# Performance work log

Hardware: AMD Instinct MI355X
Metric: run time of the kernel (lower is better)

Reference implementation:

```python
import jax, jax.numpy as jnp
import numpy as np
import math

L_SIDE = 32           # one_side_length = ceil(sqrt(L)), L = 32**2
NDIM = 16             # args.ndim (SSM state size)
N_SSM = 16            # args.n_ssm
DIRS = 4              # args.directions_amount
EMBED = 1024          # embed_dim
KD = DIRS * N_SSM     # kernel_dim = 64
CDIM = EMBED * DIRS   # C_dimensions = 4096
H = EMBED // N_SSM    # 64 (channels per ssm)
R2 = 16               # expansion terms per kernel position
R = L_SIDE * L_SIDE * R2
V = 2 * L_SIDE        # vander power dim (power_dim = kernel_dim_arg*2)
BSZ = 8
SEQ = L_SIDE * L_SIDE


def _build_one_matrix():
    # Mimics CoeffCalculator.whole_as_one: for each of d=2 flow axes and each
    # of R expansion terms, the 4 A-factor rows are one-hot selectors over the
    # V power basis, and the 5th (B) row holds an integer coefficient in one of
    # the first two columns (selecting B1 or B2).
    rng = np.random.default_rng(0)
    M = np.zeros((2, 5, R, V), dtype=np.float32)
    di = np.arange(2)[:, None]
    ri = np.arange(R)[None, :]
    for a in range(4):
        idx = rng.integers(0, V, size=(2, R))
        M[di, a, ri, idx] = 1.0
    col = rng.integers(0, 2, size=(2, R))
    coef = rng.integers(1, 5, size=(2, R)).astype(np.float32)
    M[di, 4, ri, col] = coef
    return jnp.asarray(M)


def setup_inputs() -> dict:
    key = jax.random.key(0)
    ks = jax.random.split(key, 7)
    return {
        "x": jax.random.normal(ks[0], (SEQ, BSZ, EMBED), jnp.float32),
        "A": jax.random.normal(ks[1], (4, KD, NDIM), jnp.float32) * 0.2,
        "B1": jax.random.normal(ks[2], (KD, NDIM), jnp.float32) * 0.2,
        "B2": jax.random.normal(ks[3], (KD, NDIM), jnp.float32) * 0.2,
        "C1": jax.random.normal(ks[4], (CDIM, NDIM), jnp.float32),
        "C2": jax.random.normal(ks[5], (CDIM, NDIM), jnp.float32),
        "omega": jax.random.normal(ks[6], (EMBED,), jnp.float32),
        "one_matrix": _build_one_matrix(),
    }


def _compute_kernel(A, B1, B2, C1, C2, one_matrix, dtype):
    scale = 1.0 / math.sqrt(NDIM)
    # _calc_coeffs: sigmoid on A, B
    As = jax.nn.sigmoid(A)                                  # (4, KD, NDIM)
    pw = jnp.arange(V, dtype=dtype)
    # torch.linalg.vander: increasing powers 0..V-1 -> (4, V, KD, NDIM)
    A_vals = jnp.transpose(As[..., None] ** pw, (0, 3, 1, 2))
    Bs = jax.nn.sigmoid(jnp.stack([B1, B2], 0))             # (2, KD, NDIM)
    Bpad = jnp.zeros((V, KD, NDIM), dtype).at[:2].set(Bs)   # pad to V rows
    vals = jnp.concatenate([A_vals, Bpad[None]], 0)         # (5, V, KD, NDIM)
    # 'd a R V, a V k n -> d a R k n' then product over the 5 factors
    prod = jnp.einsum('drv,vkn->drkn', one_matrix[:, 0], vals[0])
    for a in range(1, 5):
        prod = prod * jnp.einsum('drv,vkn->drkn', one_matrix[:, a], vals[a])
    # sum over r2 expansion terms per kernel position
    w = prod.reshape(2, SEQ, R2, KD, NDIM).sum(2)           # (2, SEQ, KD, NDIM)
    C = jnp.stack([C1, C2], 0) * scale                      # (2, CDIM, NDIM)
    Cr = C.reshape(2, H, KD, NDIM)
    k = jnp.einsum('dpkn,dhkn->phk', w, Cr).reshape(L_SIDE, L_SIDE, CDIM)
    # boundary scaling (first row/col x2, corner net x1)
    k = k.at[0, :, :].multiply(2.0)
    k = k.at[:, 0, :].multiply(2.0)
    k = k.at[0, 0, :].divide(4.0)
    return k


def reference(x, A, B1, B2, C1, C2, omega, one_matrix):
    k = _compute_kernel(A, B1, B2, C1, C2, one_matrix, x.dtype)
    # channel layout (H, dir, n_ssm) -> per-direction (EMBED,) kernels
    kd = k.reshape(L_SIDE, L_SIDE, H, DIRS, N_SSM)
    kd = jnp.transpose(kd, (3, 2, 4, 0, 1)).reshape(DIRS, EMBED, L_SIDE, L_SIDE)
    # 4-corner scans: flip kernel per direction; conv is linear so sum kernels
    ksum = kd[0] + kd[1, :, ::-1, :] + kd[2, :, :, ::-1] + kd[3, :, ::-1, ::-1]
    residual = x * omega                                    # 'L B D, D -> L B D'
    xg = jnp.transpose(x, (1, 2, 0)).reshape(BSZ, EMBED, L_SIDE, L_SIDE)
    s = 2 * L_SIDE
    xf = jnp.fft.rfft2(xg, s=(s, s))                        # (B, D, s, s//2+1)
    kf = jnp.fft.rfft2(ksum, s=(s, s))
    y = jnp.fft.irfft2(xf * kf, s=(s, s))[..., :L_SIDE, :L_SIDE]
    y = jnp.transpose(y.reshape(BSZ, EMBED, SEQ), (2, 0, 1))  # back to (L, B, D)
    return y + residual
```

## Files before the change

kernel.cpp:

```cpp
#include <hip/hip_runtime.h>
#include <stdint.h>


typedef __attribute__((ext_vector_type(8))) short short8;
typedef __attribute__((ext_vector_type(4))) float f32x4;

__device__ inline uint16_t f2bf(float f) {
    uint32_t u = __float_as_uint(f);
    uint32_t r = (u + 0x7FFFu + ((u >> 16) & 1u)) >> 16;
    return (uint16_t)r;
}
__device__ inline float bf2f(uint16_t v) {
    return __uint_as_float((uint32_t)v << 16);
}
__device__ inline uint32_t packbf(float a, float b) {
    return (uint32_t)f2bf(a) | ((uint32_t)f2bf(b) << 16);
}

__global__ __launch_bounds__(256) void k_pre(const float* __restrict__ x,
                                             uint16_t* __restrict__ xtb,
                                             const float* __restrict__ A,
                                             const float* __restrict__ B1,
                                             const float* __restrict__ B2,
                                             float* __restrict__ LAg,
                                             float* __restrict__ SBg) {
    __shared__ __align__(16) float shf[32 * 129];
    int bx = blockIdx.x;
    int t = threadIdx.x;

    if (bx < 2048) {
        int u = bx & 31, e0 = ((bx >> 5) & 31) * 32, r0 = (bx >> 10) * 128;
        {
            int c = t & 7, a = t >> 3;
            const float* src = x + (size_t)(u * 256 + r0) * 1024 + e0 + c * 4;
            #pragma unroll
            for (int qq = 0; qq < 4; ++qq) {
                int r = qq * 32 + a;
                float4 v = *(const float4*)(src + (size_t)r * 1024);
                shf[(c * 4 + 0) * 129 + r] = v.x;
                shf[(c * 4 + 1) * 129 + r] = v.y;
                shf[(c * 4 + 2) * 129 + r] = v.z;
                shf[(c * 4 + 3) * 129 + r] = v.w;
            }
        }
        __syncthreads();
        {
            int e_local = t >> 3, b = t & 7;
            const float* row = shf + e_local * 129;
            int v0 = r0 >> 3;
            uint32_t pk[8];
            #pragma unroll
            for (int k2 = 0; k2 < 8; ++k2)
                pk[k2] = packbf(row[(2 * k2) * 8 + b], row[(2 * k2 + 1) * 8 + b]);
            uint16_t* dst = xtb + (size_t)(e0 + e_local) * 8192 + u * 256 + b * 32 + v0;
            *(uint4*)dst       = make_uint4(pk[0], pk[1], pk[2], pk[3]);
            *(uint4*)(dst + 8) = make_uint4(pk[4], pk[5], pk[6], pk[7]);
        }
    } else {
        int i = bx - 2048;
        int e = t * 4;
        if (i < 4) {
            float4 v = *(const float4*)(A + i * 1024 + e);
            float4 o;
            o.x = -log2f(1.0f + expf(-v.x));
            o.y = -log2f(1.0f + expf(-v.y));
            o.z = -log2f(1.0f + expf(-v.z));
            o.w = -log2f(1.0f + expf(-v.w));
            *(float4*)(LAg + i * 1024 + e) = o;
        } else {
            const float* Bs = (i == 4) ? B1 : B2;
            float4 v = *(const float4*)(Bs + e);
            float4 o;
            o.x = 1.0f / (1.0f + expf(-v.x));
            o.y = 1.0f / (1.0f + expf(-v.y));
            o.z = 1.0f / (1.0f + expf(-v.z));
            o.w = 1.0f / (1.0f + expf(-v.w));
            *(float4*)(SBg + (i - 4) * 1024 + e) = o;
        }
    }
}

__global__ __launch_bounds__(256) void k_w(const float* __restrict__ om,
                                           const float* __restrict__ LAg,
                                           const float* __restrict__ SBg,
                                           float* __restrict__ w) {
    __shared__ float ff[2][16][4];
    __shared__ float cf[2][16][2];
    int p = blockIdx.x;
    int t = threadIdx.x;
    {
        int row_id = t >> 1, h = t & 1;
        int d = row_id >> 6, a = (row_id >> 4) & 3, r2 = row_id & 15;
        const float* src = om + ((size_t)(d * 5 + a) * 16384 + p * 16 + r2) * 64 + h * 32;
        float s = 0.0f;
        #pragma unroll
        for (int q = 0; q < 8; ++q) {
            float4 v = *(const float4*)(src + q * 4);
            float jb = (float)(h * 32 + q * 4);
            s = __builtin_fmaf(v.x, jb,
                __builtin_fmaf(v.y, jb + 1.0f,
                __builtin_fmaf(v.z, jb + 2.0f,
                __builtin_fmaf(v.w, jb + 3.0f, s))));
        }
        s += __shfl_xor(s, 1);
        if (h == 0) ff[d][r2][a] = s;
        if (t < 32) {
            int dd = t >> 4, rr = t & 15;
            const float* c = om + ((size_t)(dd * 5 + 4) * 16384 + p * 16 + rr) * 64;
            cf[dd][rr][0] = c[0];
            cf[dd][rr][1] = c[1];
        }
    }
    __syncthreads();

    int d = t >> 7;
    int j0 = (t & 127) * 8;
    float L0[8], L1[8], L2[8], L3[8], B0v[8], B1v[8], acc[8];
    #pragma unroll
    for (int a = 0; a < 4; ++a) {
        float* La = (a == 0) ? L0 : (a == 1) ? L1 : (a == 2) ? L2 : L3;
        float4 u0 = *(const float4*)(LAg + a * 1024 + j0);
        float4 u1 = *(const float4*)(LAg + a * 1024 + j0 + 4);
        La[0] = u0.x; La[1] = u0.y; La[2] = u0.z; La[3] = u0.w;
        La[4] = u1.x; La[5] = u1.y; La[6] = u1.z; La[7] = u1.w;
    }
    {
        float4 u0 = *(const float4*)(SBg + j0);
        float4 u1 = *(const float4*)(SBg + j0 + 4);
        float4 v0 = *(const float4*)(SBg + 1024 + j0);
        float4 v1 = *(const float4*)(SBg + 1024 + j0 + 4);
        B0v[0] = u0.x; B0v[1] = u0.y; B0v[2] = u0.z; B0v[3] = u0.w;
        B0v[4] = u1.x; B0v[5] = u1.y; B0v[6] = u1.z; B0v[7] = u1.w;
        B1v[0] = v0.x; B1v[1] = v0.y; B1v[2] = v0.z; B1v[3] = v0.w;
        B1v[4] = v1.x; B1v[5] = v1.y; B1v[6] = v1.z; B1v[7] = v1.w;
    }
    #pragma unroll
    for (int jj = 0; jj < 8; ++jj) acc[jj] = 0.0f;

    #pragma unroll
    for (int r2 = 0; r2 < 16; ++r2) {
        float f0 = ff[d][r2][0];
        float f1 = ff[d][r2][1];
        float f2 = ff[d][r2][2];
        float f3 = ff[d][r2][3];
        float c0 = cf[d][r2][0];
        float c1 = cf[d][r2][1];
        #pragma unroll
        for (int jj = 0; jj < 8; ++jj) {
            float ex = __builtin_fmaf(f3, L3[jj],
                       __builtin_fmaf(f2, L2[jj],
                       __builtin_fmaf(f1, L1[jj], f0 * L0[jj])));
            float bs = __builtin_fmaf(c1, B1v[jj], c0 * B0v[jj]);
            acc[jj] = __builtin_fmaf(exp2f(ex), bs, acc[jj]);
        }
    }
    float* dst = w + (size_t)(d * 1024 + p) * 1024 + j0;
    *(float4*)(dst)     = make_float4(acc[0], acc[1], acc[2], acc[3]);
    *(float4*)(dst + 4) = make_float4(acc[4], acc[5], acc[6], acc[7]);
}

__global__ __launch_bounds__(256) void k_kd(const float* __restrict__ w,
                                            const float* __restrict__ C1,
                                            const float* __restrict__ C2,
                                            uint16_t* __restrict__ kd4b) {
    __shared__ float Wl[128 * 33];
    __shared__ float Ctl[32 * 65];
    int kap = blockIdx.x;
    int p0 = blockIdx.y * 128;
    int dir = kap >> 4, m = kap & 15;
    int t = threadIdx.x;

    {
        int off = (t & 3) * 4;
        #pragma unroll
        for (int rep = 0; rep < 4; ++rep) {
            int row_id = rep * 64 + (t >> 2);
            int d = row_id >> 7, pp = row_id & 127;
            const float* src = w + ((size_t)(d * 1024 + p0 + pp) * 64 + kap) * 16 + off;
            float4 v = *(const float4*)src;
            float* dstl = Wl + pp * 33 + d * 16 + off;
            dstl[0] = v.x; dstl[1] = v.y; dstl[2] = v.z; dstl[3] = v.w;
        }
    }
    if (t < 128) {
        int d = t >> 6, h = t & 63;
        const float* Cd = d ? C2 : C1;
        const float* src = Cd + (size_t)(h * 64 + kap) * 16;
        #pragma unroll
        for (int q = 0; q < 16; ++q)
            Ctl[(d * 16 + q) * 65 + h] = src[q] * 0.25f;
    }
    __syncthreads();

    int ph = t & 15, hq = t >> 4;
    int pl = ph * 8, h0 = hq * 4;
    float acc[8][4];
    #pragma unroll
    for (int i = 0; i < 8; ++i)
        { acc[i][0] = acc[i][1] = acc[i][2] = acc[i][3] = 0.0f; }

    for (int k = 0; k < 32; ++k) {
        float c0 = Ctl[k * 65 + h0 + 0];
        float c1 = Ctl[k * 65 + h0 + 1];
        float c2 = Ctl[k * 65 + h0 + 2];
        float c3 = Ctl[k * 65 + h0 + 3];
        #pragma unroll
        for (int i = 0; i < 8; ++i) {
            float wv = Wl[(pl + i) * 33 + k];
            acc[i][0] += wv * c0; acc[i][1] += wv * c1;
            acc[i][2] += wv * c2; acc[i][3] += wv * c3;
        }
    }
    #pragma unroll
    for (int j = 0; j < 4; ++j) {
        int h = h0 + j;
        uint32_t pk[4];
        #pragma unroll
        for (int qq = 0; qq < 4; ++qq) {
            float v0, v1;
            #pragma unroll
            for (int z = 0; z < 2; ++z) {
                int p = p0 + pl + qq * 2 + z;
                int ii = p >> 5, jj = p & 31;
                float f = ((ii == 0) != (jj == 0)) ? 2.0f : 1.0f;
                float val = acc[qq * 2 + z][j] * f;
                if (z == 0) v0 = val; else v1 = val;
            }
            pk[qq] = packbf(v0, v1);
        }
        uint16_t* dst = kd4b + ((size_t)(dir * 1024 + h * 16 + m)) * 1024 + p0 + pl;
        *(uint4*)dst = make_uint4(pk[0], pk[1], pk[2], pk[3]);
    }
}

__global__ __launch_bounds__(256) void k_conv(const uint16_t* __restrict__ xtb,
                                              const uint16_t* __restrict__ kd4b,
                                              uint16_t* __restrict__ ytb) {
    __shared__ __align__(16) char smem[24576 + 16384];
    const int KROW = 768;
    const int SROW = 96;
    char* xtl = smem + 24576;

    int e = blockIdx.x;
    int t = threadIdx.x;
    int lane = t & 63, wv = t >> 6;
    int n = lane & 15, q = lane >> 4, nn = n & 7;

    {
        f32x4 z = {0.f, 0.f, 0.f, 0.f};
        #pragma unroll
        for (int k = 0; k < 6; ++k)
            *(f32x4*)(smem + (t + k * 256) * 16) = z;
    }
    {
        const uint4* src = (const uint4*)(xtb + (size_t)e * 8192);
        #pragma unroll
        for (int r = 0; r < 4; ++r) {
            uint4 v = src[r * 256 + t];
            *(uint4*)(xtl + (r * 256 + t) * 16) = v;
        }
    }
    int pi = t >> 3, pj = (t & 7) * 4;
    float s0, s1, s2, s3;
    {
        const uint16_t* b0 = kd4b + (size_t)e * 1024;
        ushort4 a0 = *(const ushort4*)(b0 + pi * 32 + pj);
        ushort4 a1 = *(const ushort4*)(b0 + (1 << 20) + (31 - pi) * 32 + pj);
        ushort4 a2 = *(const ushort4*)(b0 + (2 << 20) + pi * 32 + (28 - pj));
        ushort4 a3 = *(const ushort4*)(b0 + (3 << 20) + (31 - pi) * 32 + (28 - pj));
        s0 = bf2f(a0.x) + bf2f(a1.x) + bf2f(a2.w) + bf2f(a3.w);
        s1 = bf2f(a0.y) + bf2f(a1.y) + bf2f(a2.z) + bf2f(a3.z);
        s2 = bf2f(a0.z) + bf2f(a1.z) + bf2f(a2.y) + bf2f(a3.y);
        s3 = bf2f(a0.w) + bf2f(a1.w) + bf2f(a2.x) + bf2f(a3.x);
    }
    __syncthreads();

    {
        uint16_t k0 = f2bf(s0), k1 = f2bf(s1), k2 = f2bf(s2), k3 = f2bf(s3);
        #pragma unroll
        for (int s = 0; s < 8; ++s) {
            uint16_t* row = (uint16_t*)(smem + pi * KROW + s * SROW);
            int c = 31 + s - pj;
            row[c]     = k0;
            row[c - 1] = k1;
            row[c - 2] = k2;
            row[c - 3] = k3;
        }
    }
    __syncthreads();

    int A0 = n - 8 * q;
    int A1 = A0 + 16;
    int sh1 = (A1 + 9) & 7;
    int off1 = sh1 * SROW + (31 + sh1 - A1) * 2;
    int off0;
    if (A0 >= -8) {
        int sh0 = (A0 + 9) & 7;
        off0 = sh0 * SROW + (31 + sh0 - A0) * 2;
    } else {
        off0 = 80;
    }
    int boff = nn * 64 + q * 16;

    short8 Breg[16];
    #pragma unroll
    for (int u = 0; u < 16; ++u)
        Breg[u] = *(const short8*)(xtl + u * 512 + boff);

    f32x4 acc0[8], acc1[8];
    #pragma unroll
    for (int ii = 0; ii < 8; ++ii) {
        acc0[ii] = (f32x4){0.f, 0.f, 0.f, 0.f};
        acc1[ii] = (f32x4){0.f, 0.f, 0.f, 0.f};
    }

    #pragma unroll
    for (int dd = 0; dd < 4; ++dd) {
        if (dd <= wv) {
            const char* krow = smem + (wv - dd) * KROW;
            short8 a0 = *(const short8*)(krow + off0);
            short8 a1 = *(const short8*)(krow + off1);
            #pragma unroll
            for (int ii = 0; ii < 8; ++ii) {
                short8 bb = (ii < 4) ? Breg[dd + 4 * ii]
                                     : *(const short8*)(xtl + (dd + 4 * ii) * 512 + boff);
                acc0[ii] = __builtin_amdgcn_mfma_f32_16x16x32_bf16(a0, bb, acc0[ii], 0, 0, 0);
                acc1[ii] = __builtin_amdgcn_mfma_f32_16x16x32_bf16(a1, bb, acc1[ii], 0, 0, 0);
            }
        }
    }
    #pragma unroll
    for (int g = 1; g <= 7; ++g) {
        #pragma unroll
        for (int dd = 0; dd < 4; ++dd) {
            const char* krow = smem + (wv + 4 * g - 3 + dd) * KROW;
            short8 a0 = *(const short8*)(krow + off0);
            short8 a1 = *(const short8*)(krow + off1);
            #pragma unroll
            for (int ii = g; ii < 8; ++ii) {
                int u = 4 * (ii - g) + 3 - dd;
                short8 bb = (ii - g < 4) ? Breg[u]
                                         : *(const short8*)(xtl + u * 512 + boff);
                acc0[ii] = __builtin_amdgcn_mfma_f32_16x16x32_bf16(a0, bb, acc0[ii], 0, 0, 0);
                acc1[ii] = __builtin_amdgcn_mfma_f32_16x16x32_bf16(a1, bb, acc1[ii], 0, 0, 0);
            }
        }
    }

    if (n < 8) {
        uint16_t* base = ytb + ((size_t)(n * 1024 + e)) * 1024 + q * 4;
        #pragma unroll
        for (int ii = 0; ii < 8; ++ii) {
            int i = wv + 4 * ii;
            uint2 w0 = make_uint2(packbf(acc0[ii][0], acc0[ii][1]),
                                  packbf(acc0[ii][2], acc0[ii][3]));
            uint2 w1 = make_uint2(packbf(acc1[ii][0], acc1[ii][1]),
                                  packbf(acc1[ii][2], acc1[ii][3]));
            *(uint2*)(base + i * 32)      = w0;
            *(uint2*)(base + i * 32 + 16) = w1;
        }
    }
}

__global__ __launch_bounds__(256) void k_t2(const uint16_t* __restrict__ ytb,
                                            const float* __restrict__ x,
                                            const float* __restrict__ omega,
                                            float* __restrict__ out) {
    __shared__ float lds[32 * 130];
    int e0 = blockIdx.x * 32, p0 = blockIdx.y * 128, b = blockIdx.z;
    int t = threadIdx.x;
    {
        int a = t >> 3, c = t & 7;
        const uint16_t* src = ytb + (size_t)(b * 1024 + e0 + a) * 1024 + p0;
        float* dst = lds + a * 130;
        #pragma unroll
        for (int rep = 0; rep < 2; ++rep) {
            int off = (c + rep * 8) * 8;
            uint4 v = *(const uint4*)(src + off);
            uint32_t ww[4] = {v.x, v.y, v.z, v.w};
            #pragma unroll
            for (int k = 0; k < 4; ++k) {
                float2 f;
                f.x = bf2f((uint16_t)(ww[k] & 0xFFFFu));
                f.y = bf2f((uint16_t)(ww[k] >> 16));
                *(float2*)(dst + off + k * 2) = f;
            }
        }
    }
    __syncthreads();
    int pl = t >> 1, eh = (t & 1) * 16;
    int p = p0 + pl;
    const float* xs = x + ((size_t)(p * 8 + b)) * 1024 + e0 + eh;
    float* os = out + ((size_t)(p * 8 + b)) * 1024 + e0 + eh;
    #pragma unroll
    for (int qq = 0; qq < 4; ++qq) {
        float4 xv = *(const float4*)(xs + qq * 4);
        int eb = eh + qq * 4;
        float4 ov;
        ov.x = lds[(eb + 0) * 130 + pl] + xv.x * omega[e0 + eb + 0];
        ov.y = lds[(eb + 1) * 130 + pl] + xv.y * omega[e0 + eb + 1];
        ov.z = lds[(eb + 2) * 130 + pl] + xv.z * omega[e0 + eb + 2];
        ov.w = lds[(eb + 3) * 130 + pl] + xv.w * omega[e0 + eb + 3];
        *(float4*)(os + qq * 4) = ov;
    }
}

extern "C" void kernel_launch(void* const* d_in, const int* in_sizes, int n_in,
                              void* d_out, int out_size, void* d_ws, size_t ws_size,
                              hipStream_t stream) {
    (void)in_sizes; (void)n_in; (void)out_size; (void)ws_size;
    const float* x   = (const float*)d_in[0];
    const float* A   = (const float*)d_in[1];
    const float* B1  = (const float*)d_in[2];
    const float* B2  = (const float*)d_in[3];
    const float* C1  = (const float*)d_in[4];
    const float* C2  = (const float*)d_in[5];
    const float* omg = (const float*)d_in[6];
    const float* om  = (const float*)d_in[7];
    float* out = (float*)d_out;

    float* ws  = (float*)d_ws;
    uint16_t* xtb  = (uint16_t*)ws;
    uint16_t* kd4b = (uint16_t*)(ws + 4194304);
    uint16_t* ytb  = (uint16_t*)(ws + 6291456);
    float* w       = ws + 10485760;
    float* LAg     = ws + 4194304 + 65536;
    float* SBg     = ws + 4194304 + 69632;

    k_pre <<<2054, 256, 0, stream>>>(x, xtb, A, B1, B2, LAg, SBg);
    k_w   <<<1024, 256, 0, stream>>>(om, LAg, SBg, w);
    k_kd  <<<dim3(64, 8), 256, 0, stream>>>(w, C1, C2, kd4b);
    k_conv<<<1024, 256, 0, stream>>>(xtb, kd4b, ytb);
    k_t2  <<<dim3(32, 8, 8), 256, 0, stream>>>(ytb, x, omg, out);
}
```

Measured before the change: 189.7 us.

## Pack two output rows per MFMA tile using all 16 columns in conv

Reworks the MFMA mapping in the direct 2D convolution kernel. Each 16-column B tile now carries two output rows, one per half of the lanes (8 batch columns each), where before only 8 of the 16 columns held useful data. This halves the number of accumulators and MFMA calls per wave and removes the register-cached B fragments. In exchange, every B fragment is now read from LDS on each use, with extra pointer selects that substitute a zero row for out-of-range taps.

```diff
diff --git a/kernel.cpp b/kernel.cpp
--- a/kernel.cpp
+++ b/kernel.cpp
@@ -244,7 +244,7 @@
     int e = blockIdx.x;
     int t = threadIdx.x;
     int lane = t & 63, wv = t >> 6;
-    int n = lane & 15, q = lane >> 4, nn = n & 7;
+    int n = lane & 15, q = lane >> 4, nn = n & 7, hi = n >> 3;
 
     {
         f32x4 z = {0.f, 0.f, 0.f, 0.f};
@@ -301,63 +301,68 @@
         off0 = 80;
     }
     int boff = nn * 64 + q * 16;
-
-    short8 Breg[16];
-    #pragma unroll
-    for (int u = 0; u < 16; ++u)
-        Breg[u] = *(const short8*)(xtl + u * 512 + boff);
-
-    f32x4 acc0[8], acc1[8];
-    #pragma unroll
-    for (int ii = 0; ii < 8; ++ii) {
+    const char* zptr = smem + 80;
+
+    f32x4 acc0[4], acc1[4];
+    #pragma unroll
+    for (int ii = 0; ii < 4; ++ii) {
         acc0[ii] = (f32x4){0.f, 0.f, 0.f, 0.f};
         acc1[ii] = (f32x4){0.f, 0.f, 0.f, 0.f};
     }
 
     #pragma unroll
-    for (int dd = 0; dd < 4; ++dd) {
-        if (dd <= wv) {
-            const char* krow = smem + (wv - dd) * KROW;
+    for (int j = 0; j < 8; ++j) {
+        if (j <= 2 * wv + 1) {
+            const char* krow = smem + j * KROW;
             short8 a0 = *(const short8*)(krow + off0);
             short8 a1 = *(const short8*)(krow + off1);
-            #pragma unroll
-            for (int ii = 0; ii < 8; ++ii) {
-                short8 bb = (ii < 4) ? Breg[dd + 4 * ii]
-                                     : *(const short8*)(xtl + (dd + 4 * ii) * 512 + boff);
+            {
+                int u = 2 * wv + hi - j;
+                const char* bp = (u >= 0) ? (xtl + u * 512 + boff) : zptr;
+                short8 bb = *(const short8*)bp;
+                acc0[0] = __builtin_amdgcn_mfma_f32_16x16x32_bf16(a0, bb, acc0[0], 0, 0, 0);
+                acc1[0] = __builtin_amdgcn_mfma_f32_16x16x32_bf16(a1, bb, acc1[0], 0, 0, 0);
+            }
+            #pragma unroll
+            for (int ii = 1; ii < 4; ++ii) {
+                int u = 2 * wv + 8 * ii + hi - j;
+                short8 bb = *(const short8*)(xtl + u * 512 + boff);
                 acc0[ii] = __builtin_amdgcn_mfma_f32_16x16x32_bf16(a0, bb, acc0[ii], 0, 0, 0);
                 acc1[ii] = __builtin_amdgcn_mfma_f32_16x16x32_bf16(a1, bb, acc1[ii], 0, 0, 0);
             }
         }
     }
     #pragma unroll
-    for (int g = 1; g <= 7; ++g) {
-        #pragma unroll
-        for (int dd = 0; dd < 4; ++dd) {
-            const char* krow = smem + (wv + 4 * g - 3 + dd) * KROW;
+    for (int b = 1; b <= 3; ++b) {
+        #pragma unroll
+        for (int m = 0; m < 8; ++m) {
+            int di = 2 * wv + 8 * b - 6 + m;
+            const char* krow = smem + di * KROW;
             short8 a0 = *(const short8*)(krow + off0);
             short8 a1 = *(const short8*)(krow + off1);
             #pragma unroll
-            for (int ii = g; ii < 8; ++ii) {
-                int u = 4 * (ii - g) + 3 - dd;
-                short8 bb = (ii - g < 4) ? Breg[u]
-                                         : *(const short8*)(xtl + u * 512 + boff);
+            for (int ii = b; ii < 4; ++ii) {
+                int u = 8 * (ii - b) + 6 + hi - m;
+                const char* bp = ((ii == b) && (m == 7) && (hi == 0))
+                                     ? zptr : (xtl + u * 512 + boff);
+                short8 bb = *(const short8*)bp;
                 acc0[ii] = __builtin_amdgcn_mfma_f32_16x16x32_bf16(a0, bb, acc0[ii], 0, 0, 0);
                 acc1[ii] = __builtin_amdgcn_mfma_f32_16x16x32_bf16(a1, bb, acc1[ii], 0, 0, 0);
             }
         }
     }
 
-    if (n < 8) {
-        uint16_t* base = ytb + ((size_t)(n * 1024 + e)) * 1024 + q * 4;
-        #pragma unroll
-        for (int ii = 0; ii < 8; ++ii) {
-            int i = wv + 4 * ii;
+    {
+        uint16_t* base = ytb + ((size_t)(nn * 1024 + e)) * 1024 + q * 4;
+        #pragma unroll
+        for (int ii = 0; ii < 4; ++ii) {
+            int ro = 2 * wv + 8 * ii + hi;
             uint2 w0 = make_uint2(packbf(acc0[ii][0], acc0[ii][1]),
                                   packbf(acc0[ii][2], acc0[ii][3]));
             uint2 w1 = make_uint2(packbf(acc1[ii][0], acc1[ii][1]),
                                   packbf(acc1[ii][2], acc1[ii][3]));
-            *(uint2*)(base + i * 32)      = w0;
-            *(uint2*)(base + i * 32 + 16) = w1;
+            *(uint2*)(base + ro * 32)      = w0;
+            *(uint2*)(base + ro * 32 + 16) = w1;
         }
     }
 }
```

Measured after the change: 187.5 us. Within noise of the previous version (-1.2%).
